# Performance work log

Hardware: AMD Instinct MI355X
Metric: run time of the kernel (lower is better)

## Reference

```python
import jax, jax.numpy as jnp
import numpy as np

B, L, H, D = 2, 2048, 16, 64


def setup_inputs() -> dict:
    key = jax.random.key(0)
    k1, k2, k3, k4 = jax.random.split(key, 4)
    query_states = jax.random.normal(k1, (B, L, H, D), dtype=jnp.float32)
    key_states = jax.random.normal(k2, (B, L, H, D), dtype=jnp.float32)
    # per-head linear feature maps (LinearFeatureMap parameters)
    Wq = jax.random.normal(k3, (H, D, D), dtype=jnp.float32)
    Wk = jax.random.normal(k4, (H, D, D), dtype=jnp.float32)
    return {"query_states": query_states, "key_states": key_states, "Wq": Wq, "Wk": Wk}


def reference(query_states, key_states, Wq, Wk):
    # per-head linear feature map: [B,L,H,D] x [H,D,E] -> [B,L,H,E]
    q = jnp.einsum('blhd,hde->blhe', query_states, Wq)
    k = jnp.einsum('blhd,hde->blhe', key_states, Wk)
    # kernelized attention scores: [B,H,L,S]
    attn = jnp.einsum('blhd,bshd->bhls', q, k)
    # sum-normalization over keys (non-softmax normalizer)
    attn = attn / jnp.sum(attn, axis=-1, keepdims=True)
    return attn
```

## Files before the change

kernel.cpp:

```cpp
#include <hip/hip_runtime.h>
#include <stdint.h>

#define NB 2
#define NL 2048
#define NH 16
#define ND 64

typedef __attribute__((ext_vector_type(8))) short short8;
typedef __attribute__((ext_vector_type(4))) float f32x4;
typedef __attribute__((ext_vector_type(4))) unsigned short ushort4v;

__device__ __forceinline__ unsigned short f2bf_rne(float x) {
    union { float f; unsigned int u; } v; v.f = x;
    unsigned int r = v.u + 0x7fffu + ((v.u >> 16) & 1u);
    return (unsigned short)(r >> 16);
}
__device__ __forceinline__ float bf2f(unsigned short b) {
    union { unsigned int u; float f; } v; v.u = ((unsigned int)b) << 16;
    return v.f;
}

__global__ __launch_bounds__(256) void pre_kernel(const float* __restrict__ query,
                                                  const float* __restrict__ key,
                                                  const float* __restrict__ Wq,
                                                  const float* __restrict__ Wk,
                                                  unsigned short* __restrict__ qbh,
                                                  unsigned short* __restrict__ qbl,
                                                  unsigned short* __restrict__ kbh,
                                                  unsigned short* __restrict__ kbl,
                                                  double* __restrict__ part) {
    __shared__ __align__(16) char lds_raw[16384 + 34816];
    const int blk = blockIdx.x;
    const int t = threadIdx.x;

    if (blk < 1024) {
        const bool isq = blk < 512;
        const int pb = isq ? blk : blk - 512;
        const float* x = isq ? query : key;
        const float* W = isq ? Wq : Wk;
        unsigned short* ph = isq ? qbh : kbh;
        unsigned short* pl = isq ? qbl : kbl;
        float* Wlds = (float*)lds_raw;
        float* xs = (float*)(lds_raw + 16384);

        const int lc = pb & 15;
        const int h = (pb >> 4) & 15;
        const int b = pb >> 8;
        const int l0 = lc * 128;

        {
            const float4* src = (const float4*)(W + (size_t)h * ND * ND);
#pragma unroll
            for (int i = 0; i < 4; ++i)
                ((float4*)Wlds)[t + 256 * i] = src[t + 256 * i];
        }
        {
#pragma unroll
            for (int i = 0; i < 8; ++i) {
                const int idx = t + 256 * i;
                const int r = idx >> 4, c = idx & 15;
                const float4 v = *(const float4*)(x + (((size_t)b * NL + l0 + r) * NH + h) * ND + c * 4);
                *(float4*)&xs[r * 68 + c * 4] = v;
            }
        }
        __syncthreads();

        const int e4 = (t & 15) * 4;
        const int rg = t >> 4;
        float acc[8][4] = {};
        for (int d = 0; d < ND; ++d) {
            const float4 w4 = *(const float4*)&Wlds[d * ND + e4];
#pragma unroll
            for (int it = 0; it < 8; ++it) {
                const float xv = xs[(rg + it * 16) * 68 + d];
                acc[it][0] += xv * w4.x; acc[it][1] += xv * w4.y;
                acc[it][2] += xv * w4.z; acc[it][3] += xv * w4.w;
            }
        }

        unsigned short* phh = ph + ((size_t)(b * NH + h) * NL + l0) * ND;
        unsigned short* pll = pl + ((size_t)(b * NH + h) * NL + l0) * ND;
#pragma unroll
        for (int it = 0; it < 8; ++it) {
            const int r = rg + it * 16;
            const int ep = e4 ^ ((r & 7) << 3);
            ushort4v hv, lv;
#pragma unroll
            for (int j = 0; j < 4; ++j) {
                const unsigned short hb = f2bf_rne(acc[it][j]);
                hv[j] = hb;
                lv[j] = f2bf_rne(acc[it][j] - bf2f(hb));
            }
            *(ushort4v*)&phh[(size_t)r * ND + ep] = hv;
            *(ushort4v*)&pll[(size_t)r * ND + ep] = lv;
        }
    } else {
        double (*red)[64] = (double(*)[64])lds_raw;
        const int blk2 = blk - 1024;
        const int chunk = blk2 & 15, bh = blk2 >> 4;
        const int b = bh >> 4, h = bh & 15;
        const int e = t & 63, sub = t >> 6;
        const float* base = key + ((size_t)b * NL * NH + h) * ND + e;
        double acc = 0.0;
        const int s0 = chunk * 128 + sub * 32;
        for (int s = s0; s < s0 + 32; ++s)
            acc += (double)base[(size_t)s * (NH * ND)];
        red[sub][e] = acc;
        __syncthreads();
        if (t < 64) {
            const double s2 = red[0][t] + red[1][t] + red[2][t] + red[3][t];
            part[(size_t)blk2 * 64 + t] = s2;
        }
    }
}

__global__ __launch_bounds__(256) void den_kernel(const float* __restrict__ xq,
                                                  const double* __restrict__ part,
                                                  const float* __restrict__ Wq,
                                                  const float* __restrict__ Wk,
                                                  float* __restrict__ invden) {
    __shared__ double xs[ND], ks[ND], vs[ND];
    const int bh = blockIdx.x;
    const int b = bh >> 4, h = bh & 15;
    const int t = threadIdx.x;
    if (t < 64) {
        double a = 0.0;
#pragma unroll
        for (int c = 0; c < 16; ++c) a += part[((size_t)bh * 16 + c) * 64 + t];
        xs[t] = a;
    }
    __syncthreads();
    if (t < 64) {
        double acc = 0.0;
        const float* wk = Wk + (size_t)h * ND * ND + t;
        for (int d = 0; d < ND; ++d) acc += xs[d] * (double)wk[(size_t)d * ND];
        ks[t] = acc;
    }
    __syncthreads();
    if (t < 64) {
        double acc = 0.0;
        const float* wq = Wq + (size_t)h * ND * ND + (size_t)t * ND;
        for (int e = 0; e < ND; ++e) acc += (double)wq[e] * ks[e];
        vs[t] = acc;
    }
    __syncthreads();
    const int l = blockIdx.y * 256 + t;
    const float* xp = xq + (((size_t)b * NL + l) * NH + h) * ND;
    double acc = 0.0;
#pragma unroll 8
    for (int d = 0; d < ND; ++d) acc += (double)xp[d] * vs[d];
    invden[(size_t)bh * NL + l] = (float)(1.0 / acc);
}

__global__ __launch_bounds__(512, 1) void attn_kernel(const unsigned short* __restrict__ qbh,
                                                      const unsigned short* __restrict__ qbl,
                                                      const unsigned short* __restrict__ kbh,
                                                      const unsigned short* __restrict__ kbl,
                                                      const float* __restrict__ invden,
                                                      float* __restrict__ out) {
    __shared__ unsigned short kwbuf[8][2][2][1024];
    __shared__ f32x4 obuf[8][512];
    const int strip = blockIdx.x;
    const int bh = blockIdx.y;
    const int t = threadIdx.x;
    const int w = t >> 6, ln = t & 63;
    const int fr = ln & 15, g = ln >> 4;
    const int swz = (fr & 7) << 4;
    const int cofs0 = (g << 4) ^ swz;
    const int cofs1 = (64 | (g << 4)) ^ swz;

    const size_t pan = (size_t)bh * NL * ND;
    const unsigned short* kh_p = kbh + pan;
    const unsigned short* kl_p = kbl + pan;
    const char* qh_pb = (const char*)(qbh + pan);
    const char* ql_pb = (const char*)(qbl + pan);
    const int lbase = strip * 256 + w * 32;

    short8 qf00, qf01, qf10, qf11, qg00, qg01, qg10, qg11;
    {
        const size_t r0 = (size_t)(lbase + fr) * 128;
        const size_t r1 = (size_t)(lbase + 16 + fr) * 128;
        qf00 = *(const short8*)(qh_pb + r0 + cofs0);
        qf01 = *(const short8*)(qh_pb + r0 + cofs1);
        qf10 = *(const short8*)(ql_pb + r0 + cofs0);
        qf11 = *(const short8*)(ql_pb + r0 + cofs1);
        qg00 = *(const short8*)(qh_pb + r1 + cofs0);
        qg01 = *(const short8*)(qh_pb + r1 + cofs1);
        qg10 = *(const short8*)(ql_pb + r1 + cofs0);
        qg11 = *(const short8*)(ql_pb + r1 + cofs1);
    }
    const float inv0 = invden[(size_t)bh * NL + lbase + fr];
    const float inv1 = invden[(size_t)bh * NL + lbase + 16 + fr];
    asm volatile("s_waitcnt vmcnt(0)" ::: "memory");
    __builtin_amdgcn_sched_barrier(0);

#define STAGE(c, buf)                                                                               \
    {                                                                                               \
        _Pragma("unroll")                                                                           \
        for (int u = 0; u < 2; ++u) {                                                               \
            __builtin_amdgcn_global_load_lds(                                                       \
                (const __attribute__((address_space(1))) unsigned int*)(kh_p + (size_t)(c) * 1024 + u * 512 + ln * 8), \
                (__attribute__((address_space(3))) unsigned int*)(&kwbuf[w][buf][0][u * 512]), 16, 0, 0); \
        }                                                                                           \
        _Pragma("unroll")                                                                           \
        for (int u = 0; u < 2; ++u) {                                                               \
            __builtin_amdgcn_global_load_lds(                                                       \
                (const __attribute__((address_space(1))) unsigned int*)(kl_p + (size_t)(c) * 1024 + u * 512 + ln * 8), \
                (__attribute__((address_space(3))) unsigned int*)(&kwbuf[w][buf][1][u * 512]), 16, 0, 0); \
        }                                                                                           \
    }

#define WAITN(n)                                            \
    asm volatile("s_waitcnt vmcnt(" #n ")" ::: "memory");   \
    __builtin_amdgcn_sched_barrier(0)

#define LDS_FENCE()                                         \
    asm volatile("s_waitcnt lgkmcnt(0)" ::: "memory");      \
    __builtin_amdgcn_sched_barrier(0)

#define COMPUTE(b, cc)                                                                              \
    {                                                                                               \
        const char* kh_b = (const char*)&kwbuf[w][b][0][0];                                         \
        const char* kl_b = (const char*)&kwbuf[w][b][1][0];                                         \
        const int soff = fr * 128;                                                                  \
        const short8 kh0 = *(const short8*)(kh_b + soff + cofs0);                                   \
        const short8 kh1 = *(const short8*)(kh_b + soff + cofs1);                                   \
        const short8 kl0 = *(const short8*)(kl_b + soff + cofs0);                                   \
        const short8 kl1 = *(const short8*)(kl_b + soff + cofs1);                                   \
        {                                                                                           \
            f32x4 a = (f32x4){0.f, 0.f, 0.f, 0.f};                                                  \
            a = __builtin_amdgcn_mfma_f32_16x16x32_bf16(kh0, qf00, a, 0, 0, 0);                     \
            a = __builtin_amdgcn_mfma_f32_16x16x32_bf16(kh0, qf10, a, 0, 0, 0);                     \
            a = __builtin_amdgcn_mfma_f32_16x16x32_bf16(kl0, qf00, a, 0, 0, 0);                     \
            a = __builtin_amdgcn_mfma_f32_16x16x32_bf16(kh1, qf01, a, 0, 0, 0);                     \
            a = __builtin_amdgcn_mfma_f32_16x16x32_bf16(kh1, qf11, a, 0, 0, 0);                     \
            a = __builtin_amdgcn_mfma_f32_16x16x32_bf16(kl1, qf01, a, 0, 0, 0);                     \
            a[0] *= inv0; a[1] *= inv0; a[2] *= inv0; a[3] *= inv0;                                 \
            obuf[w][fr * 16 + (((cc) * 4 + g) ^ fr)] = a;                                           \
        }                                                                                           \
        {                                                                                           \
            f32x4 a = (f32x4){0.f, 0.f, 0.f, 0.f};                                                  \
            a = __builtin_amdgcn_mfma_f32_16x16x32_bf16(kh0, qg00, a, 0, 0, 0);                     \
            a = __builtin_amdgcn_mfma_f32_16x16x32_bf16(kh0, qg10, a, 0, 0, 0);                     \
            a = __builtin_amdgcn_mfma_f32_16x16x32_bf16(kl0, qg00, a, 0, 0, 0);                     \
            a = __builtin_amdgcn_mfma_f32_16x16x32_bf16(kh1, qg01, a, 0, 0, 0);                     \
            a = __builtin_amdgcn_mfma_f32_16x16x32_bf16(kh1, qg11, a, 0, 0, 0);                     \
            a = __builtin_amdgcn_mfma_f32_16x16x32_bf16(kl1, qg01, a, 0, 0, 0);                     \
            a[0] *= inv1; a[1] *= inv1; a[2] *= inv1; a[3] *= inv1;                                 \
            obuf[w][(16 + fr) * 16 + (((cc) * 4 + g) ^ fr)] = a;                                    \
        }                                                                                           \
    }

#define FLUSH(c4)                                                                                   \
    {                                                                                               \
        f32x4 ov[8];                                                                                \
        _Pragma("unroll")                                                                           \
        for (int k8 = 0; k8 < 8; ++k8) {                                                            \
            const int row = k8 * 4 + (ln >> 4);                                                     \
            ov[k8] = obuf[w][row * 16 + ((ln & 15) ^ (row & 15))];                                  \
        }                                                                                           \
        LDS_FENCE();                                                                                \
        _Pragma("unroll")                                                                           \
        for (int k8 = 0; k8 < 8; ++k8) {                                                            \
            const int row = k8 * 4 + (ln >> 4);                                                     \
            *(f32x4*)(out + ((size_t)bh * NL + lbase + row) * NL + (c4) * 64 + (ln & 15) * 4) = ov[k8]; \
        }                                                                                           \
    }

    STAGE(0, 0);
    STAGE(1, 1);

    WAITN(4); COMPUTE(0, 0); LDS_FENCE(); STAGE(2, 0);
    WAITN(4); COMPUTE(1, 1); LDS_FENCE(); STAGE(3, 1);
    WAITN(4); COMPUTE(0, 2); LDS_FENCE(); STAGE(4, 0);
    WAITN(4); COMPUTE(1, 3); LDS_FENCE(); STAGE(5, 1);
    FLUSH(0);

    for (int c4 = 1; c4 <= 30; ++c4) {
        const int c = c4 * 4;
        WAITN(12); COMPUTE(0, 0); LDS_FENCE(); STAGE(c + 2, 0);
        WAITN(12); COMPUTE(1, 1); LDS_FENCE(); STAGE(c + 3, 1);
        WAITN(4);  COMPUTE(0, 2); LDS_FENCE(); STAGE(c + 4, 0);
        WAITN(4);  COMPUTE(1, 3); LDS_FENCE(); STAGE(c + 5, 1);
        FLUSH(c4);
    }

    WAITN(12); COMPUTE(0, 0); LDS_FENCE(); STAGE(126, 0);
    WAITN(12); COMPUTE(1, 1); LDS_FENCE(); STAGE(127, 1);
    WAITN(4);  COMPUTE(0, 2); LDS_FENCE();
    WAITN(0);  COMPUTE(1, 3); LDS_FENCE();
    FLUSH(31);

#undef STAGE
#undef WAITN
#undef LDS_FENCE
#undef COMPUTE
#undef FLUSH
}

extern "C" void kernel_launch(void* const* d_in, const int* in_sizes, int n_in,
                              void* d_out, int out_size, void* d_ws, size_t ws_size,
                              hipStream_t stream) {
    const float* query = (const float*)d_in[0];
    const float* key   = (const float*)d_in[1];
    const float* Wq    = (const float*)d_in[2];
    const float* Wk    = (const float*)d_in[3];
    float* out = (float*)d_out;

    const size_t npan = (size_t)NB * NH * NL * ND;
    char* ws = (char*)d_ws;
    unsigned short* qbh = (unsigned short*)(ws);
    unsigned short* qbl = (unsigned short*)(ws + 1 * npan * 2);
    unsigned short* kbh = (unsigned short*)(ws + 2 * npan * 2);
    unsigned short* kbl = (unsigned short*)(ws + 3 * npan * 2);
    double* part  = (double*)(ws + 4 * npan * 2);
    float* invden = (float*)(ws + 4 * npan * 2 + 262144);

    pre_kernel<<<1536, 256, 0, stream>>>(query, key, Wq, Wk, qbh, qbl, kbh, kbl, part);
    den_kernel<<<dim3(NB * NH, NL / 256), 256, 0, stream>>>(query, part, Wq, Wk, invden);
    attn_kernel<<<dim3(8, NB * NH), 512, 0, stream>>>(qbh, qbl, kbh, kbl, invden, out);
}
```

Baseline: 178.9 us.

## Fuse per-row denominator into attention kernel and compute head vector once

The old den_kernel recomputed the per-head vector (Wq·Wk·sum of keys) in every one of its row-strip blocks, then wrote inverse denominators to global memory. That step is now split. A tiny prep kernel computes the head vector once per batch-head. The attention kernel then computes each row's FP64 dot product and reciprocal into shared memory at its start. This removes redundant matvecs and the invden global round-trip, but adds a serial FP64 dot loop to the start of every attention block, ahead of the tile pipeline.

```diff
diff --git a/kernel.cpp b/kernel.cpp
--- a/kernel.cpp
+++ b/kernel.cpp
@@ -114,54 +114,49 @@
     }
 }
 
-__global__ __launch_bounds__(256) void den_kernel(const float* __restrict__ xq,
-                                                  const double* __restrict__ part,
+__global__ __launch_bounds__(64) void prep_kernel(const double* __restrict__ part,
                                                   const float* __restrict__ Wq,
                                                   const float* __restrict__ Wk,
-                                                  float* __restrict__ invden) {
-    __shared__ double xs[ND], ks[ND], vs[ND];
+                                                  double* __restrict__ v) {
+    __shared__ double xs[ND], ks[ND];
     const int bh = blockIdx.x;
-    const int b = bh >> 4, h = bh & 15;
+    const int h = bh & 15;
     const int t = threadIdx.x;
-    if (t < 64) {
+    {
         double a = 0.0;
 #pragma unroll
         for (int c = 0; c < 16; ++c) a += part[((size_t)bh * 16 + c) * 64 + t];
         xs[t] = a;
     }
     __syncthreads();
-    if (t < 64) {
+    {
         double acc = 0.0;
         const float* wk = Wk + (size_t)h * ND * ND + t;
         for (int d = 0; d < ND; ++d) acc += xs[d] * (double)wk[(size_t)d * ND];
         ks[t] = acc;
     }
     __syncthreads();
-    if (t < 64) {
+    {
         double acc = 0.0;
         const float* wq = Wq + (size_t)h * ND * ND + (size_t)t * ND;
         for (int e = 0; e < ND; ++e) acc += (double)wq[e] * ks[e];
-        vs[t] = acc;
-    }
-    __syncthreads();
-    const int l = blockIdx.y * 256 + t;
-    const float* xp = xq + (((size_t)b * NL + l) * NH + h) * ND;
-    double acc = 0.0;
-#pragma unroll 8
-    for (int d = 0; d < ND; ++d) acc += (double)xp[d] * vs[d];
-    invden[(size_t)bh * NL + l] = (float)(1.0 / acc);
-}
-
-__global__ __launch_bounds__(512, 1) void attn_kernel(const unsigned short* __restrict__ qbh,
+        v[(size_t)bh * ND + t] = acc;
+    }
+}
+
+__global__ __launch_bounds__(512, 1) void attn_kernel(const float* __restrict__ query,
+                                                      const double* __restrict__ vden,
+                                                      const unsigned short* __restrict__ qbh,
                                                       const unsigned short* __restrict__ qbl,
                                                       const unsigned short* __restrict__ kbh,
                                                       const unsigned short* __restrict__ kbl,
-                                                      const float* __restrict__ invden,
                                                       float* __restrict__ out) {
     __shared__ unsigned short kwbuf[8][2][2][1024];
     __shared__ f32x4 obuf[8][512];
+    __shared__ float invs[256];
     const int strip = blockIdx.x;
     const int bh = blockIdx.y;
+    const int b = bh >> 4, h = bh & 15;
     const int t = threadIdx.x;
     const int w = t >> 6, ln = t & 63;
     const int fr = ln & 15, g = ln >> 4;
@@ -175,6 +170,18 @@
     const char* qh_pb = (const char*)(qbh + pan);
     const char* ql_pb = (const char*)(qbl + pan);
     const int lbase = strip * 256 + w * 32;
+
+    {
+        if (ln < 32) {
+            const int l = lbase + ln;
+            const float* xp = query + (((size_t)b * NL + l) * NH + h) * ND;
+            const double* vp = vden + (size_t)bh * ND;
+            double acc = 0.0;
+#pragma unroll 8
+            for (int d = 0; d < ND; ++d) acc += (double)xp[d] * vp[d];
+            invs[w * 32 + ln] = (float)(1.0 / acc);
+        }
+    }
 
     short8 qf00, qf01, qf10, qf11, qg00, qg01, qg10, qg11;
     {
@@ -189,8 +196,8 @@
         qg10 = *(const short8*)(ql_pb + r1 + cofs0);
         qg11 = *(const short8*)(ql_pb + r1 + cofs1);
     }
-    const float inv0 = invden[(size_t)bh * NL + lbase + fr];
-    const float inv1 = invden[(size_t)bh * NL + lbase + 16 + fr];
+    const float inv0 = invs[w * 32 + fr];
+    const float inv1 = invs[w * 32 + 16 + fr];
     asm volatile("s_waitcnt vmcnt(0)" ::: "memory");
     __builtin_amdgcn_sched_barrier(0);
 
@@ -314,9 +321,9 @@
     unsigned short* kbh = (unsigned short*)(ws + 2 * npan * 2);
     unsigned short* kbl = (unsigned short*)(ws + 3 * npan * 2);
     double* part  = (double*)(ws + 4 * npan * 2);
-    float* invden = (float*)(ws + 4 * npan * 2 + 262144);
+    double* vden  = (double*)(ws + 4 * npan * 2 + 262144);
 
     pre_kernel<<<1536, 256, 0, stream>>>(query, key, Wq, Wk, qbh, qbl, kbh, kbl, part);
-    den_kernel<<<dim3(NB * NH, NL / 256), 256, 0, stream>>>(query, part, Wq, Wk, invden);
-    attn_kernel<<<dim3(8, NB * NH), 512, 0, stream>>>(qbh, qbl, kbh, kbl, invden, out);
-}
+    prep_kernel<<<NB * NH, 64, 0, stream>>>(part, Wq, Wk, vden);
+    attn_kernel<<<dim3(8, NB * NH), 512, 0, stream>>>(query, vden, qbh, qbl, kbh, kbl, out);
+}
```

New measurement: 175.7 us. Within noise of the previous version (-1.8%).
